# Performance work log

Measured on AMD Instinct MI355X. Metric: run time of the kernel, lower is better.

## Reference

```python
import jax, jax.numpy as jnp
import numpy as np

D_MODEL, D_EDGE, D_STRUCT = 128, 64, 8
N, E, B = 50000, 800000, 1

def _lin(key, din, dout):
    kw, kb = jax.random.split(key)
    s = 1.0 / np.sqrt(din)
    return (jax.random.uniform(kw, (din, dout), jnp.float32, -s, s),
            jax.random.uniform(kb, (dout,), jnp.float32, -s, s))

def setup_inputs() -> dict:
    key = jax.random.key(0)
    ks = jax.random.split(key, 16)
    H = jax.random.normal(ks[0], (B, N, D_MODEL), jnp.float32)
    xyz = jax.random.normal(ks[1], (B, N, 3), jnp.float32)
    edge_index = jax.random.randint(ks[2], (2, E), 0, N, jnp.int64)
    edge_struct = jax.random.normal(ks[3], (E, D_STRUCT), jnp.float32)
    edge_rest_lengths = jax.random.uniform(ks[4], (E,), jnp.float32)
    We1, be1 = _lin(ks[5], 2 * D_MODEL + 2 + D_STRUCT, D_EDGE)
    We2, be2 = _lin(ks[6], D_EDGE, D_EDGE)
    Wg1, bg1 = _lin(ks[7], 2 + D_STRUCT, 32)
    Wg2, bg2 = _lin(ks[8], 32, 1)
    Wn1, bn1 = _lin(ks[9], D_MODEL + D_EDGE, 2 * D_MODEL)
    Wn2, bn2 = _lin(ks[10], 2 * D_MODEL, D_MODEL)
    ln_g = jnp.ones((D_MODEL,), jnp.float32)
    ln_b = jnp.zeros((D_MODEL,), jnp.float32)
    return dict(H=H, xyz=xyz, edge_index=edge_index, edge_struct=edge_struct,
                edge_rest_lengths=edge_rest_lengths,
                We1=We1, be1=be1, We2=We2, be2=be2,
                Wg1=Wg1, bg1=bg1, Wg2=Wg2, bg2=bg2,
                Wn1=Wn1, bn1=bn1, Wn2=Wn2, bn2=bn2,
                ln_g=ln_g, ln_b=ln_b)

def reference(H, xyz, edge_index, edge_struct, edge_rest_lengths,
              We1, be1, We2, be2, Wg1, bg1, Wg2, bg2,
              Wn1, bn1, Wn2, bn2, ln_g, ln_b):
    Bn, Nn, d = H.shape
    i, j = edge_index[0], edge_index[1]
    # edge geometry
    diff = xyz[:, i, :] - xyz[:, j, :]                      # (B,E,3)
    dist2 = jnp.sum(diff * diff, axis=-1, keepdims=True)    # (B,E,1)
    dist = jnp.sqrt(dist2 + 1e-9)
    rest = edge_rest_lengths.reshape(1, -1, 1)
    delta = (dist - rest) / (rest + 1e-9)
    struct = jnp.broadcast_to(edge_struct[None], (Bn, edge_struct.shape[0], edge_struct.shape[1]))
    # edge message MLP
    Hi, Hj = H[:, i, :], H[:, j, :]
    e_in = jnp.concatenate([Hi, Hj, dist2, delta, struct], axis=-1)  # (B,E,2d+2+ds)
    e = jax.nn.silu(e_in @ We1 + be1)
    e_msg = jax.nn.silu(e @ We2 + be2)                       # (B,E,d_edge)
    # gate
    g_in = jnp.concatenate([dist2, delta, struct], axis=-1)
    g = jax.nn.sigmoid(jax.nn.silu(g_in @ Wg1 + bg1) @ Wg2 + bg2)  # (B,E,1)
    e_msg = e_msg * g
    # scatter-add aggregate to destination node i
    agg = jnp.zeros((Bn, Nn, e_msg.shape[-1]), H.dtype).at[:, i, :].add(e_msg)
    # node MLP (dropout is identity at eval) + residual + LayerNorm
    n_in = jnp.concatenate([H, agg], axis=-1)
    upd = jax.nn.silu(n_in @ Wn1 + bn1) @ Wn2 + bn2
    x = H + upd
    mu = jnp.mean(x, axis=-1, keepdims=True)
    var = jnp.mean((x - mu) ** 2, axis=-1, keepdims=True)
    return (x - mu) / jnp.sqrt(var + 1e-5) * ln_g + ln_b
```

## Files before the change

kernel.cpp:

```cpp
#include <hip/hip_runtime.h>
#include <stdint.h>

#define N_NODES 50000
#define N_EDGES 800000
#define NODE_TILES 782

#define SE   72
#define SW2  72
#define SPQ  136
#define SN1  200
#define SN2  264
#define SH1  264
#define ATS  32
#define MSTR 68

#define EC_GRID 962
#define EC_CHUNK 13

#define SCAN_B 98

typedef short bf16x8 __attribute__((ext_vector_type(8)));
typedef short short4v __attribute__((ext_vector_type(4)));
typedef unsigned short ushort8 __attribute__((ext_vector_type(8)));
typedef float f32x4  __attribute__((ext_vector_type(4)));

static __device__ __forceinline__ unsigned short f2bf(float f) {
  unsigned int x = __float_as_uint(f);
  unsigned int r = (x + 0x7fffu + ((x >> 16) & 1u)) >> 16;
  return (unsigned short)r;
}
static __device__ __forceinline__ float bf2f(unsigned short u) {
  return __uint_as_float(((unsigned int)u) << 16);
}
static __device__ __forceinline__ float silu_f(float x) {
  return x * __builtin_amdgcn_rcpf(1.0f + __expf(-x));
}
static __device__ __forceinline__ float sigmoid_f(float x) {
  return __builtin_amdgcn_rcpf(1.0f + __expf(-x));
}
static __device__ __forceinline__ unsigned int cvt_pk_bf16(float lo, float hi) {
  unsigned int r;
  asm("v_cvt_pk_bf16_f32 %0, %1, %2" : "=v"(r) : "v"(lo), "v"(hi));
  return r;
}
static __device__ __forceinline__ bf16x8 pack8(float4 u, float4 v) {
  bf16x8 w;
  w[0] = (short)f2bf(u.x); w[1] = (short)f2bf(u.y);
  w[2] = (short)f2bf(u.z); w[3] = (short)f2bf(u.w);
  w[4] = (short)f2bf(v.x); w[5] = (short)f2bf(v.y);
  w[6] = (short)f2bf(v.z); w[7] = (short)f2bf(v.w);
  return w;
}

__global__ void prep_hist(
    const int* __restrict__ eidx,
    const float* __restrict__ We1, const float* __restrict__ be1,
    const float* __restrict__ We2,
    const float* __restrict__ Wn1, const float* __restrict__ Wn2,
    unsigned short* __restrict__ WpqT, unsigned short* __restrict__ We2T,
    unsigned short* __restrict__ Wn1T, unsigned short* __restrict__ Wn2T,
    unsigned short* __restrict__ WrT,
    int* __restrict__ cnt)
{
  const int gid = blockIdx.x * 256 + threadIdx.x;
  const int gsz = gridDim.x * 256;
  for (int i = gid; i < 128 * SPQ; i += gsz) {
    int n = i / SPQ, k = i % SPQ;
    unsigned short v = 0;
    if (k < 128) v = (n < 64) ? f2bf(We1[k * 64 + n]) : f2bf(We1[(128 + k) * 64 + (n - 64)]);
    WpqT[i] = v;
  }
  for (int i = gid; i < 64 * SW2; i += gsz) {
    int n = i / SW2, k = i % SW2;
    We2T[i] = (k < 64) ? f2bf(We2[k * 64 + n]) : (unsigned short)0;
  }
  for (int i = gid; i < 256 * SN1; i += gsz) {
    int n = i / SN1, k = i % SN1;
    Wn1T[i] = (k < 192) ? f2bf(Wn1[k * 256 + n]) : (unsigned short)0;
  }
  for (int i = gid; i < 128 * SN2; i += gsz) {
    int n = i / SN2, k = i % SN2;
    Wn2T[i] = (k < 256) ? f2bf(Wn2[k * 128 + n]) : (unsigned short)0;
  }
  for (int i = gid; i < 64 * 32; i += gsz) {
    int n = i >> 5, k = i & 31;
    float v = 0.f;
    if (k < 2)       v = We1[256 * 64 + n];
    else if (k < 4)  v = We1[257 * 64 + n];
    else if (k < 12) v = We1[(258 + (k - 4)) * 64 + n];
    else if (k == 12) v = be1[n];
    else if (k == 13) { float w = We1[256 * 64 + n]; v = w - bf2f(f2bf(w)); }
    else if (k == 14) { float w = We1[257 * 64 + n]; v = w - bf2f(f2bf(w)); }
    else if (k == 15) { float w = be1[n];            v = w - bf2f(f2bf(w)); }
    WrT[i] = (k < 16) ? f2bf(v) : (unsigned short)0;
  }
  if (gid < N_EDGES) atomicAdd(&cnt[eidx[gid]], 1);
}

__global__ __launch_bounds__(512) void scan_local(
    const int* __restrict__ cnt, int* __restrict__ rowptr,
    int* __restrict__ bsum)
{
  __shared__ int wsum[8], woff[8];
  const int t = threadIdx.x;
  const int idx = blockIdx.x * 512 + t;
  const int lane = t & 63, wid = t >> 6;
  int c = (idx < N_NODES) ? cnt[idx] : 0;
  int v = c;
  #pragma unroll
  for (int o = 1; o < 64; o <<= 1) {
    int u = __shfl_up(v, o);
    if (lane >= o) v += u;
  }
  if (lane == 63) wsum[wid] = v;
  __syncthreads();
  if (t == 0) {
    int a = 0;
    #pragma unroll
    for (int w = 0; w < 8; ++w) { woff[w] = a; a += wsum[w]; }
    bsum[blockIdx.x] = a;
  }
  __syncthreads();
  if (idx < N_NODES) rowptr[idx] = woff[wid] + (v - c);
}

__global__ __launch_bounds__(128) void scan_mid(
    const int* __restrict__ bsum, int* __restrict__ boff)
{
  __shared__ int ws[2];
  const int t = threadIdx.x;
  const int lane = t & 63, wid = t >> 6;
  int c = (t < SCAN_B) ? bsum[t] : 0;
  int v = c;
  #pragma unroll
  for (int o = 1; o < 64; o <<= 1) {
    int u = __shfl_up(v, o);
    if (lane >= o) v += u;
  }
  if (lane == 63) ws[wid] = v;
  __syncthreads();
  int add = (wid == 1) ? ws[0] : 0;
  if (t < SCAN_B) boff[t] = add + (v - c);
}

__global__ __launch_bounds__(512) void scan_add(
    const int* __restrict__ rowptr, const int* __restrict__ boff,
    int* __restrict__ cursor)
{
  const int idx = blockIdx.x * 512 + threadIdx.x;
  if (idx < N_NODES) cursor[idx] = rowptr[idx] + boff[blockIdx.x];
}

__global__ void fill_kernel(const int* __restrict__ eidx,
                            int* __restrict__ cursor, int* __restrict__ order)
{
  int e = blockIdx.x * 256 + threadIdx.x;
  if (e < N_EDGES) {
    int d = eidx[e];
    int pos = atomicAdd(&cursor[d], 1);
    order[pos] = e;
  }
}

__global__ void reorder_kernel(
    const int* __restrict__ eidx, const float* __restrict__ xyz,
    const float* __restrict__ estruct, const float* __restrict__ erest,
    const int* __restrict__ order,
    const float* __restrict__ Wg1, const float* __restrict__ bg1,
    const float* __restrict__ Wg2, const float* __restrict__ bg2,
    float4* __restrict__ metaA, unsigned short* __restrict__ sst,
    int* __restrict__ in_s)
{
  int s = blockIdx.x * 256 + threadIdx.x;
  if (s >= N_EDGES) return;
  int e = order[s];
  int i = eidx[e], j = eidx[N_EDGES + e];
  float dx = xyz[i * 3 + 0] - xyz[j * 3 + 0];
  float dy = xyz[i * 3 + 1] - xyz[j * 3 + 1];
  float dz = xyz[i * 3 + 2] - xyz[j * 3 + 2];
  float d2 = dx * dx + dy * dy + dz * dz;
  float dist = sqrtf(d2 + 1e-9f);
  float rest = erest[e];
  float dl = (dist - rest) / (rest + 1e-9f);
  float4 s0 = *(const float4*)&estruct[e * 8];
  float4 s1 = *(const float4*)&estruct[e * 8 + 4];
  float st[8] = {s0.x, s0.y, s0.z, s0.w, s1.x, s1.y, s1.z, s1.w};
  float gsum = 0.f;
  #pragma unroll
  for (int h = 0; h < 32; ++h) {
    float a = bg1[h] + d2 * Wg1[0 * 32 + h] + dl * Wg1[1 * 32 + h];
    #pragma unroll
    for (int c = 0; c < 8; ++c) a += st[c] * Wg1[(2 + c) * 32 + h];
    gsum += silu_f(a) * Wg2[h];
  }
  float g = sigmoid_f(gsum + bg2[0]);
  metaA[s] = make_float4(d2, dl, g, __int_as_float(j));
  ushort8 w;
  #pragma unroll
  for (int c = 0; c < 8; ++c) w[c] = f2bf(st[c]);
  *(ushort8*)&sst[(long)s * 8] = w;
  in_s[s] = i;
}

__global__ __launch_bounds__(256, 2) void pq_kernel(
    const float* __restrict__ H, const unsigned short* __restrict__ WpqT,
    unsigned short* __restrict__ P, unsigned short* __restrict__ Q,
    unsigned short* __restrict__ Hbf)
{
  __shared__ unsigned short As[64 * SPQ];
  __shared__ unsigned short Ws[128 * SPQ];

  const int tid  = threadIdx.x;
  const int lane = tid & 63;
  const int wv   = tid >> 6;
  const int lr   = lane & 15;
  const int lq   = lane >> 4;
  const int m0   = wv * 16;
  const int n0   = blockIdx.x * 64;

  for (int i = tid * 8; i < 128 * SPQ; i += 256 * 8)
    *(bf16x8*)&Ws[i] = *(const bf16x8*)&WpqT[i];
  {
    int le = tid >> 2, q = tid & 3;
    int node = n0 + le; if (node >= N_NODES) node = N_NODES - 1;
    const float* src = H + (long)node * 128 + q * 32;
    unsigned short* dst = &As[le * SPQ + q * 32];
    #pragma unroll
    for (int c = 0; c < 32; c += 8) {
      float4 u = *(const float4*)(src + c);
      float4 v = *(const float4*)(src + c + 4);
      *(bf16x8*)(dst + c) = pack8(u, v);
    }
  }
  __syncthreads();

  for (int idx = tid * 8; idx < 64 * 128; idx += 256 * 8) {
    int row = idx >> 7, col = idx & 127;
    *(bf16x8*)&Hbf[((long)n0 + row) * 128 + col] = *(const bf16x8*)&As[row * SPQ + col];
  }

  f32x4 zero4 = {0.f, 0.f, 0.f, 0.f};
  f32x4 acc[8];
  #pragma unroll
  for (int f = 0; f < 8; ++f) acc[f] = zero4;
  #pragma unroll
  for (int s = 0; s < 4; ++s) {
    int kb = s * 32 + lq * 8;
    bf16x8 a = *(const bf16x8*)&As[(m0 + lr) * SPQ + kb];
    #pragma unroll
    for (int f = 0; f < 8; ++f) {
      bf16x8 b = *(const bf16x8*)&Ws[(f * 16 + lr) * SPQ + kb];
      acc[f] = __builtin_amdgcn_mfma_f32_16x16x32_bf16(a, b, acc[f], 0, 0, 0);
    }
  }
  #pragma unroll
  for (int f = 0; f < 8; ++f) {
    #pragma unroll
    for (int r = 0; r < 4; ++r) {
      int node = n0 + m0 + lq * 4 + r;
      if (node < N_NODES) {
        if (f < 4) P[(long)node * 64 + f * 16 + lr] = f2bf(acc[f][r]);
        else       Q[(long)node * 64 + (f - 4) * 16 + lr] = f2bf(acc[f][r]);
      }
    }
  }
}

__global__ __launch_bounds__(256, 4) void edge_compute(
    const unsigned short* __restrict__ P, const unsigned short* __restrict__ Q,
    const int* __restrict__ in_s,
    const float4* __restrict__ metaA, const unsigned short* __restrict__ sst,
    const unsigned short* __restrict__ We2T, const float* __restrict__ be2,
    const unsigned short* __restrict__ WrT,
    float* __restrict__ agg)
{
  __shared__ unsigned short W2s[64 * SW2];
  __shared__ unsigned short Es [4 * 16 * SE];
  __shared__ unsigned short At [4 * 16 * ATS];
  __shared__ float          Ms [4 * 16 * MSTR];

  const int tid  = threadIdx.x;
  const int lane = tid & 63;
  const int wv   = tid >> 6;
  const int lr   = lane & 15;
  const int lq   = lane >> 4;

  for (int i = tid * 8; i < 64 * SW2; i += 256 * 8)
    *(bf16x8*)&W2s[i] = *(const bf16x8*)&We2T[i];

  unsigned short* Es_w = &Es[wv * 16 * SE];
  unsigned short* At_w = &At[wv * 16 * ATS];
  float*          Ms_w = &Ms[wv * 16 * MSTR];

  if (lane < 16) {
    ushort8 z;
    #pragma unroll
    for (int c = 0; c < 8; ++c) z[c] = 0;
    *(ushort8*)&At_w[lane * ATS + 16] = z;
    *(ushort8*)&At_w[lane * ATS + 24] = z;
  }

  bf16x8 aWr[4];
  float bias2[4][4];
  #pragma unroll
  for (int f = 0; f < 4; ++f) {
    aWr[f] = *(const bf16x8*)&WrT[(f * 16 + lr) * 32 + lq * 8];
    #pragma unroll
    for (int r = 0; r < 4; ++r) bias2[f][r] = be2[f * 16 + lq * 4 + r];
  }
  __syncthreads();

  const int n_tiles = N_EDGES / 16;
  const int wid = blockIdx.x * 4 + wv;
  const int t0 = wid * EC_CHUNK;
  const int t1 = (t0 + EC_CHUNK < n_tiles) ? (t0 + EC_CHUNK) : n_tiles;
  if (t0 >= n_tiles) return;

  f32x4 zero4 = {0.f, 0.f, 0.f, 0.f};
  int   cur_node   = in_s[t0 * 16];
  float acc        = 0.f;
  bool  use_atomic = true;

  for (int tile = t0; tile < t1; ++tile) {
    const int s0 = tile * 16;

    float4 mm = metaA[s0 + lr];
    int   inode = in_s[s0 + lr];
    int   jnode = __float_as_int(mm.w);
    float g     = mm.z;

    if (lane < 16) {
      ushort8 sv = *(const ushort8*)&sst[(long)(s0 + lane) * 8];
      float d2 = mm.x, dl = mm.y;
      unsigned short d2h = f2bf(d2);
      unsigned short d2l = f2bf(d2 - bf2f(d2h));
      unsigned short dlh = f2bf(dl);
      unsigned short dll = f2bf(dl - bf2f(dlh));
      ushort8 w0, w1;
      w0[0] = d2h;   w0[1] = d2l;   w0[2] = dlh;   w0[3] = dll;
      w0[4] = sv[0]; w0[5] = sv[1]; w0[6] = sv[2]; w0[7] = sv[3];
      w1[0] = sv[4]; w1[1] = sv[5]; w1[2] = sv[6]; w1[3] = sv[7];
      w1[4] = 0x3F80u; w1[5] = d2h; w1[6] = dlh;  w1[7] = 0x3F80u;
      *(ushort8*)&At_w[lane * ATS]     = w0;
      *(ushort8*)&At_w[lane * ATS + 8] = w1;
    }

    bf16x8 bA = *(const bf16x8*)&At_w[lr * ATS + lq * 8];
    f32x4 acc1[4];
    #pragma unroll
    for (int f = 0; f < 4; ++f)
      acc1[f] = __builtin_amdgcn_mfma_f32_16x16x32_bf16(aWr[f], bA, zero4, 0, 0, 0);

    const unsigned short* Pb = P + (long)inode * 64;
    const unsigned short* Qb = Q + (long)jnode * 64;
    #pragma unroll
    for (int f = 0; f < 4; ++f) {
      short4v pv = *(const short4v*)&Pb[f * 16 + lq * 4];
      short4v qv = *(const short4v*)&Qb[f * 16 + lq * 4];
      float v0 = silu_f(bf2f((unsigned short)pv[0]) + bf2f((unsigned short)qv[0]) + acc1[f][0]);
      float v1 = silu_f(bf2f((unsigned short)pv[1]) + bf2f((unsigned short)qv[1]) + acc1[f][1]);
      float v2 = silu_f(bf2f((unsigned short)pv[2]) + bf2f((unsigned short)qv[2]) + acc1[f][2]);
      float v3 = silu_f(bf2f((unsigned short)pv[3]) + bf2f((unsigned short)qv[3]) + acc1[f][3]);
      uint2 w;
      w.x = cvt_pk_bf16(v0, v1);
      w.y = cvt_pk_bf16(v2, v3);
      *(uint2*)&Es_w[lr * SE + f * 16 + lq * 4] = w;
    }

    f32x4 acc2[4];
    #pragma unroll
    for (int f = 0; f < 4; ++f) acc2[f] = zero4;
    #pragma unroll
    for (int s = 0; s < 2; ++s) {
      int kb = s * 32 + lq * 8;
      bf16x8 bE = *(const bf16x8*)&Es_w[lr * SE + kb];
      #pragma unroll
      for (int f = 0; f < 4; ++f) {
        bf16x8 aW = *(const bf16x8*)&W2s[(f * 16 + lr) * SW2 + kb];
        acc2[f] = __builtin_amdgcn_mfma_f32_16x16x32_bf16(aW, bE, acc2[f], 0, 0, 0);
      }
    }

    #pragma unroll
    for (int f = 0; f < 4; ++f) {
      f32x4 o;
      o[0] = silu_f(acc2[f][0] + bias2[f][0]) * g;
      o[1] = silu_f(acc2[f][1] + bias2[f][1]) * g;
      o[2] = silu_f(acc2[f][2] + bias2[f][2]) * g;
      o[3] = silu_f(acc2[f][3] + bias2[f][3]) * g;
      *(f32x4*)&Ms_w[lr * MSTR + f * 16 + lq * 4] = o;
    }

    #pragma unroll
    for (int e = 0; e < 16; ++e) {
      int ie = __builtin_amdgcn_readlane(inode, e);
      if (ie != cur_node) {
        if (use_atomic) atomicAdd(&agg[(long)cur_node * 64 + lane], acc);
        else            agg[(long)cur_node * 64 + lane] = acc;
        use_atomic = false;
        cur_node = ie;
        acc = 0.f;
      }
      acc += Ms_w[e * MSTR + lane];
    }
  }
  atomicAdd(&agg[(long)cur_node * 64 + lane], acc);
}

__global__ __launch_bounds__(256, 4) void node_fused_kernel(
    const float* __restrict__ H, const unsigned short* __restrict__ Hbf,
    const float* __restrict__ agg,
    const unsigned short* __restrict__ Wn1T, const float* __restrict__ bn1,
    const unsigned short* __restrict__ Wn2T, const float* __restrict__ bn2,
    const float* __restrict__ ln_g, const float* __restrict__ ln_b,
    float* __restrict__ out)
{
  __shared__ unsigned short h1t[64 * SH1];

  const int tid  = threadIdx.x;
  const int lane = tid & 63;
  const int wv   = tid >> 6;
  const int lr   = lane & 15;
  const int lq   = lane >> 4;
  const int m0   = wv * 16;
  const int n0   = blockIdx.x * 64;

  int rowa = n0 + m0 + lr;
  int rowc = rowa < N_NODES ? rowa : N_NODES - 1;

  f32x4 zero4 = {0.f, 0.f, 0.f, 0.f};
  f32x4 acc1[16];
  #pragma unroll
  for (int f = 0; f < 16; ++f) acc1[f] = zero4;
  #pragma unroll
  for (int s = 0; s < 6; ++s) {
    int kb = s * 32 + lq * 8;
    bf16x8 a;
    if (s < 4) {
      a = *(const bf16x8*)&Hbf[(long)rowa * 128 + kb];
    } else {
      const float* p = agg + (long)rowc * 64 + (kb - 128);
      float4 u = *(const float4*)p;
      float4 v = *(const float4*)(p + 4);
      a = pack8(u, v);
    }
    #pragma unroll
    for (int f = 0; f < 16; ++f) {
      bf16x8 b = *(const bf16x8*)&Wn1T[(long)(f * 16 + lr) * SN1 + kb];
      acc1[f] = __builtin_amdgcn_mfma_f32_16x16x32_bf16(a, b, acc1[f], 0, 0, 0);
    }
  }
  #pragma unroll
  for (int f = 0; f < 16; ++f) {
    float bias = bn1[f * 16 + lr];
    #pragma unroll
    for (int r = 0; r < 4; ++r)
      h1t[(m0 + lq * 4 + r) * SH1 + f * 16 + lr] = f2bf(silu_f(acc1[f][r] + bias));
  }

  f32x4 acc2[8];
  #pragma unroll
  for (int f = 0; f < 8; ++f) acc2[f] = zero4;
  #pragma unroll
  for (int s = 0; s < 8; ++s) {
    int kb = s * 32 + lq * 8;
    bf16x8 a = *(const bf16x8*)&h1t[(m0 + lr) * SH1 + kb];
    #pragma unroll
    for (int f = 0; f < 8; ++f) {
      bf16x8 b = *(const bf16x8*)&Wn2T[(long)(f * 16 + lr) * SN2 + kb];
      acc2[f] = __builtin_amdgcn_mfma_f32_16x16x32_bf16(a, b, acc2[f], 0, 0, 0);
    }
  }

  #pragma unroll
  for (int r = 0; r < 4; ++r) {
    int node = n0 + m0 + lq * 4 + r;
    int nc = node < N_NODES ? node : N_NODES - 1;
    float x[8];
    float sum = 0.f, sumsq = 0.f;
    #pragma unroll
    for (int f = 0; f < 8; ++f) {
      int n = f * 16 + lr;
      float u = acc2[f][r] + bn2[n];
      float xv = H[(long)nc * 128 + n] + u;
      x[f] = xv;
      sum += xv;
      sumsq += xv * xv;
    }
    #pragma unroll
    for (int o = 1; o < 16; o <<= 1) {
      sum   += __shfl_xor(sum, o);
      sumsq += __shfl_xor(sumsq, o);
    }
    float mu  = sum * (1.f / 128.f);
    float var = sumsq * (1.f / 128.f) - mu * mu;
    float rstd = rsqrtf(var + 1e-5f);
    if (node < N_NODES) {
      #pragma unroll
      for (int f = 0; f < 8; ++f) {
        int n = f * 16 + lr;
        out[(long)node * 128 + n] = (x[f] - mu) * rstd * ln_g[n] + ln_b[n];
      }
    }
  }
}

extern "C" void kernel_launch(void* const* d_in, const int* in_sizes, int n_in,
                              void* d_out, int out_size, void* d_ws, size_t ws_size,
                              hipStream_t stream) {
  const float* H       = (const float*)d_in[0];
  const float* xyz     = (const float*)d_in[1];
  const int*   eidx    = (const int*)d_in[2];
  const float* estruct = (const float*)d_in[3];
  const float* erest   = (const float*)d_in[4];
  const float* We1     = (const float*)d_in[5];
  const float* be1     = (const float*)d_in[6];
  const float* We2     = (const float*)d_in[7];
  const float* be2     = (const float*)d_in[8];
  const float* Wg1     = (const float*)d_in[9];
  const float* bg1     = (const float*)d_in[10];
  const float* Wg2     = (const float*)d_in[11];
  const float* bg2     = (const float*)d_in[12];
  const float* Wn1     = (const float*)d_in[13];
  const float* bn1     = (const float*)d_in[14];
  const float* Wn2     = (const float*)d_in[15];
  const float* bn2     = (const float*)d_in[16];
  const float* ln_g    = (const float*)d_in[17];
  const float* ln_b    = (const float*)d_in[18];

  char* ws = (char*)d_ws;
  float*          agg    = (float*)(ws + 0);
  unsigned short* Hbf    = (unsigned short*)(ws + 12812288);
  float4*         metaA  = (float4*)(ws + 25624576);
  unsigned short* sst    = (unsigned short*)(ws + 38424576);
  int*            in_s   = (int*)(ws + 51224576);
  int*            order  = (int*)(ws + 54424576);
  unsigned short* P      = (unsigned short*)(ws + 54424576);
  unsigned short* Qm     = (unsigned short*)(ws + 60824576);
  int*            cnt    = (int*)(ws + 67224576);
  int*            rowptr = (int*)(ws + 67424768);
  int*            cursor = (int*)(ws + 67624960);
  unsigned short* WpqT   = (unsigned short*)(ws + 67825152);
  unsigned short* We2T   = (unsigned short*)(ws + 67859968);
  unsigned short* Wn1T   = (unsigned short*)(ws + 67869184);
  unsigned short* Wn2T   = (unsigned short*)(ws + 67971584);
  unsigned short* WrT    = (unsigned short*)(ws + 68039168);
  int*            bsum   = (int*)(ws + 68043264);
  int*            boff   = (int*)(ws + 68043776);
  float* out = (float*)d_out;

  hipMemsetAsync(cnt, 0, (size_t)N_NODES * sizeof(int), stream);
  hipMemsetAsync(agg, 0, (size_t)50048 * 64 * sizeof(float), stream);

  hipLaunchKernelGGL(prep_hist, dim3(3125), dim3(256), 0, stream,
                     eidx, We1, be1, We2, Wn1, Wn2, WpqT, We2T, Wn1T, Wn2T, WrT, cnt);
  hipLaunchKernelGGL(scan_local, dim3(SCAN_B), dim3(512), 0, stream,
                     cnt, rowptr, bsum);
  hipLaunchKernelGGL(scan_mid, dim3(1), dim3(128), 0, stream,
                     bsum, boff);
  hipLaunchKernelGGL(scan_add, dim3(SCAN_B), dim3(512), 0, stream,
                     rowptr, boff, cursor);
  hipLaunchKernelGGL(fill_kernel, dim3(3125), dim3(256), 0, stream,
                     eidx, cursor, order);
  hipLaunchKernelGGL(reorder_kernel, dim3(3125), dim3(256), 0, stream,
                     eidx, xyz, estruct, erest, order,
                     Wg1, bg1, Wg2, bg2, metaA, sst, in_s);
  hipLaunchKernelGGL(pq_kernel, dim3(NODE_TILES), dim3(256), 0, stream,
                     H, WpqT, P, Qm, Hbf);
  hipLaunchKernelGGL(edge_compute, dim3(EC_GRID), dim3(256), 0, stream,
                     P, Qm, in_s, metaA, sst, We2T, be2, WrT, agg);
  hipLaunchKernelGGL(node_fused_kernel, dim3(NODE_TILES), dim3(256), 0, stream,
                     H, Hbf, agg, Wn1T, bn1, Wn2T, bn2, ln_g, ln_b, out);
}
```

Baseline: 402.0 us.

## Fuse fill into reorder, bf16 message staging, split node MLP with LDS weights

Merges the edge fill and reorder kernels so each edge computes its gate and writes directly to its CSR slot via an atomic cursor, removing the order array pass. Edge messages are staged in LDS as bf16 instead of fp32, halving shared traffic. The fused node MLP is split into two persistent kernels that keep Wn1 halves and Wn2 in LDS, with h1 round-tripped through global memory. This adds an extra global write and read of h1 and changes the edge order within each segment to be nondeterministic.

Result: faster. 389.7 us (-3.1%).

```diff
diff --git a/kernel.cpp b/kernel.cpp
--- a/kernel.cpp
+++ b/kernel.cpp
@@ -8,11 +8,10 @@
 #define SE   72
 #define SW2  72
 #define SPQ  136
-#define SN1  200
-#define SN2  264
-#define SH1  264
-#define ATS  32
-#define MSTR 68
+#define SN1  216
+#define SN2  280
+#define ATS  40
+#define MSTR 72
 
 #define EC_GRID 962
 #define EC_CHUNK 13
@@ -151,29 +150,17 @@
   if (idx < N_NODES) cursor[idx] = rowptr[idx] + boff[blockIdx.x];
 }
 
-__global__ void fill_kernel(const int* __restrict__ eidx,
-                            int* __restrict__ cursor, int* __restrict__ order)
-{
-  int e = blockIdx.x * 256 + threadIdx.x;
-  if (e < N_EDGES) {
-    int d = eidx[e];
-    int pos = atomicAdd(&cursor[d], 1);
-    order[pos] = e;
-  }
-}
-
-__global__ void reorder_kernel(
+__global__ void fill_reorder(
     const int* __restrict__ eidx, const float* __restrict__ xyz,
     const float* __restrict__ estruct, const float* __restrict__ erest,
-    const int* __restrict__ order,
+    int* __restrict__ cursor,
     const float* __restrict__ Wg1, const float* __restrict__ bg1,
     const float* __restrict__ Wg2, const float* __restrict__ bg2,
     float4* __restrict__ metaA, unsigned short* __restrict__ sst,
     int* __restrict__ in_s)
 {
-  int s = blockIdx.x * 256 + threadIdx.x;
-  if (s >= N_EDGES) return;
-  int e = order[s];
+  int e = blockIdx.x * 256 + threadIdx.x;
+  if (e >= N_EDGES) return;
   int i = eidx[e], j = eidx[N_EDGES + e];
   float dx = xyz[i * 3 + 0] - xyz[j * 3 + 0];
   float dy = xyz[i * 3 + 1] - xyz[j * 3 + 1];
@@ -194,12 +181,14 @@
     gsum += silu_f(a) * Wg2[h];
   }
   float g = sigmoid_f(gsum + bg2[0]);
-  metaA[s] = make_float4(d2, dl, g, __int_as_float(j));
+
+  int pos = atomicAdd(&cursor[i], 1);
+  metaA[pos] = make_float4(d2, dl, g, __int_as_float(j));
   ushort8 w;
   #pragma unroll
   for (int c = 0; c < 8; ++c) w[c] = f2bf(st[c]);
-  *(ushort8*)&sst[(long)s * 8] = w;
-  in_s[s] = i;
+  *(ushort8*)&sst[(long)pos * 8] = w;
+  in_s[pos] = i;
 }
 
 __global__ __launch_bounds__(256, 2) void pq_kernel(
@@ -277,7 +266,7 @@
   __shared__ unsigned short W2s[64 * SW2];
   __shared__ unsigned short Es [4 * 16 * SE];
   __shared__ unsigned short At [4 * 16 * ATS];
-  __shared__ float          Ms [4 * 16 * MSTR];
+  __shared__ unsigned short Ms [4 * 16 * MSTR];
 
   const int tid  = threadIdx.x;
   const int lane = tid & 63;
@@ -290,7 +279,7 @@
 
   unsigned short* Es_w = &Es[wv * 16 * SE];
   unsigned short* At_w = &At[wv * 16 * ATS];
-  float*          Ms_w = &Ms[wv * 16 * MSTR];
+  unsigned short* Ms_w = &Ms[wv * 16 * MSTR];
 
   if (lane < 16) {
     ushort8 z;
@@ -383,12 +372,14 @@
 
     #pragma unroll
     for (int f = 0; f < 4; ++f) {
-      f32x4 o;
-      o[0] = silu_f(acc2[f][0] + bias2[f][0]) * g;
-      o[1] = silu_f(acc2[f][1] + bias2[f][1]) * g;
-      o[2] = silu_f(acc2[f][2] + bias2[f][2]) * g;
-      o[3] = silu_f(acc2[f][3] + bias2[f][3]) * g;
-      *(f32x4*)&Ms_w[lr * MSTR + f * 16 + lq * 4] = o;
+      float o0 = silu_f(acc2[f][0] + bias2[f][0]) * g;
+      float o1 = silu_f(acc2[f][1] + bias2[f][1]) * g;
+      float o2 = silu_f(acc2[f][2] + bias2[f][2]) * g;
+      float o3 = silu_f(acc2[f][3] + bias2[f][3]) * g;
+      uint2 w;
+      w.x = cvt_pk_bf16(o0, o1);
+      w.y = cvt_pk_bf16(o2, o3);
+      *(uint2*)&Ms_w[lr * MSTR + f * 16 + lq * 4] = w;
     }
 
     #pragma unroll
@@ -401,21 +392,18 @@
         cur_node = ie;
         acc = 0.f;
       }
-      acc += Ms_w[e * MSTR + lane];
+      acc += bf2f(Ms_w[e * MSTR + lane]);
     }
   }
   atomicAdd(&agg[(long)cur_node * 64 + lane], acc);
 }
 
-__global__ __launch_bounds__(256, 4) void node_fused_kernel(
-    const float* __restrict__ H, const unsigned short* __restrict__ Hbf,
-    const float* __restrict__ agg,
+__global__ __launch_bounds__(256, 2) void h1_kernel(
+    const unsigned short* __restrict__ Hbf, const float* __restrict__ agg,
     const unsigned short* __restrict__ Wn1T, const float* __restrict__ bn1,
-    const unsigned short* __restrict__ Wn2T, const float* __restrict__ bn2,
-    const float* __restrict__ ln_g, const float* __restrict__ ln_b,
-    float* __restrict__ out)
-{
-  __shared__ unsigned short h1t[64 * SH1];
+    unsigned short* __restrict__ h1)
+{
+  __shared__ unsigned short Wl[128 * SN1];
 
   const int tid  = threadIdx.x;
   const int lane = tid & 63;
@@ -423,83 +411,119 @@
   const int lr   = lane & 15;
   const int lq   = lane >> 4;
   const int m0   = wv * 16;
-  const int n0   = blockIdx.x * 64;
-
-  int rowa = n0 + m0 + lr;
-  int rowc = rowa < N_NODES ? rowa : N_NODES - 1;
+  const int p    = blockIdx.x & 1;
+
+  for (int i = tid * 8; i < 128 * SN1; i += 256 * 8)
+    *(bf16x8*)&Wl[i] = *(const bf16x8*)&Wn1T[p * 128 * SN1 + i];
+  __syncthreads();
 
   f32x4 zero4 = {0.f, 0.f, 0.f, 0.f};
-  f32x4 acc1[16];
-  #pragma unroll
-  for (int f = 0; f < 16; ++f) acc1[f] = zero4;
-  #pragma unroll
-  for (int s = 0; s < 6; ++s) {
-    int kb = s * 32 + lq * 8;
-    bf16x8 a;
-    if (s < 4) {
-      a = *(const bf16x8*)&Hbf[(long)rowa * 128 + kb];
-    } else {
-      const float* p = agg + (long)rowc * 64 + (kb - 128);
-      float4 u = *(const float4*)p;
-      float4 v = *(const float4*)(p + 4);
-      a = pack8(u, v);
-    }
-    #pragma unroll
-    for (int f = 0; f < 16; ++f) {
-      bf16x8 b = *(const bf16x8*)&Wn1T[(long)(f * 16 + lr) * SN1 + kb];
-      acc1[f] = __builtin_amdgcn_mfma_f32_16x16x32_bf16(a, b, acc1[f], 0, 0, 0);
-    }
-  }
-  #pragma unroll
-  for (int f = 0; f < 16; ++f) {
-    float bias = bn1[f * 16 + lr];
-    #pragma unroll
-    for (int r = 0; r < 4; ++r)
-      h1t[(m0 + lq * 4 + r) * SH1 + f * 16 + lr] = f2bf(silu_f(acc1[f][r] + bias));
-  }
-
-  f32x4 acc2[8];
-  #pragma unroll
-  for (int f = 0; f < 8; ++f) acc2[f] = zero4;
-  #pragma unroll
-  for (int s = 0; s < 8; ++s) {
-    int kb = s * 32 + lq * 8;
-    bf16x8 a = *(const bf16x8*)&h1t[(m0 + lr) * SH1 + kb];
+  for (int t = blockIdx.x >> 1; t < NODE_TILES; t += 256) {
+    const int n0 = t * 64;
+    int rowa = n0 + m0 + lr;
+    int rowc = rowa < N_NODES ? rowa : N_NODES - 1;
+
+    f32x4 acc1[8];
+    #pragma unroll
+    for (int f = 0; f < 8; ++f) acc1[f] = zero4;
+    #pragma unroll
+    for (int s = 0; s < 6; ++s) {
+      int kb = s * 32 + lq * 8;
+      bf16x8 a;
+      if (s < 4) {
+        a = *(const bf16x8*)&Hbf[(long)rowa * 128 + kb];
+      } else {
+        const float* pp = agg + (long)rowc * 64 + (kb - 128);
+        float4 u = *(const float4*)pp;
+        float4 v = *(const float4*)(pp + 4);
+        a = pack8(u, v);
+      }
+      #pragma unroll
+      for (int f = 0; f < 8; ++f) {
+        bf16x8 b = *(const bf16x8*)&Wl[(f * 16 + lr) * SN1 + kb];
+        acc1[f] = __builtin_amdgcn_mfma_f32_16x16x32_bf16(a, b, acc1[f], 0, 0, 0);
+      }
+    }
     #pragma unroll
     for (int f = 0; f < 8; ++f) {
-      bf16x8 b = *(const bf16x8*)&Wn2T[(long)(f * 16 + lr) * SN2 + kb];
-      acc2[f] = __builtin_amdgcn_mfma_f32_16x16x32_bf16(a, b, acc2[f], 0, 0, 0);
-    }
-  }
-
-  #pragma unroll
-  for (int r = 0; r < 4; ++r) {
-    int node = n0 + m0 + lq * 4 + r;
-    int nc = node < N_NODES ? node : N_NODES - 1;
-    float x[8];
-    float sum = 0.f, sumsq = 0.f;
-    #pragma unroll
-    for (int f = 0; f < 8; ++f) {
-      int n = f * 16 + lr;
-      float u = acc2[f][r] + bn2[n];
-      float xv = H[(long)nc * 128 + n] + u;
-      x[f] = xv;
-      sum += xv;
-      sumsq += xv * xv;
-    }
-    #pragma unroll
-    for (int o = 1; o < 16; o <<= 1) {
-      sum   += __shfl_xor(sum, o);
-      sumsq += __shfl_xor(sumsq, o);
-    }
-    float mu  = sum * (1.f / 128.f);
-    float var = sumsq * (1.f / 128.f) - mu * mu;
-    float rstd = rsqrtf(var + 1e-5f);
-    if (node < N_NODES) {
+      int col = p * 128 + f * 16 + lr;
+      float bias = bn1[col];
+      #pragma unroll
+      for (int r = 0; r < 4; ++r) {
+        int node = n0 + m0 + lq * 4 + r;
+        h1[(long)node * 256 + col] = f2bf(silu_f(acc1[f][r] + bias));
+      }
+    }
+  }
+}
+
+__global__ __launch_bounds__(256, 2) void out_kernel(
+    const float* __restrict__ H, const unsigned short* __restrict__ h1,
+    const unsigned short* __restrict__ Wn2T, const float* __restrict__ bn2,
+    const float* __restrict__ ln_g, const float* __restrict__ ln_b,
+    float* __restrict__ out)
+{
+  __shared__ unsigned short Wl[128 * SN2];
+
+  const int tid  = threadIdx.x;
+  const int lane = tid & 63;
+  const int wv   = tid >> 6;
+  const int lr   = lane & 15;
+  const int lq   = lane >> 4;
+  const int m0   = wv * 16;
+
+  for (int i = tid * 8; i < 128 * SN2; i += 256 * 8)
+    *(bf16x8*)&Wl[i] = *(const bf16x8*)&Wn2T[i];
+  __syncthreads();
+
+  f32x4 zero4 = {0.f, 0.f, 0.f, 0.f};
+  for (int t = blockIdx.x; t < NODE_TILES; t += 512) {
+    const int n0 = t * 64;
+    int rowa = n0 + m0 + lr;
+
+    f32x4 acc2[8];
+    #pragma unroll
+    for (int f = 0; f < 8; ++f) acc2[f] = zero4;
+    #pragma unroll
+    for (int s = 0; s < 8; ++s) {
+      int kb = s * 32 + lq * 8;
+      bf16x8 a = *(const bf16x8*)&h1[(long)rowa * 256 + kb];
+      #pragma unroll
+      for (int f = 0; f < 8; ++f) {
+        bf16x8 b = *(const bf16x8*)&Wl[(f * 16 + lr) * SN2 + kb];
+        acc2[f] = __builtin_amdgcn_mfma_f32_16x16x32_bf16(a, b, acc2[f], 0, 0, 0);
+      }
+    }
+
+    #pragma unroll
+    for (int r = 0; r < 4; ++r) {
+      int node = n0 + m0 + lq * 4 + r;
+      int nc = node < N_NODES ? node : N_NODES - 1;
+      float x[8];
+      float sum = 0.f, sumsq = 0.f;
       #pragma unroll
       for (int f = 0; f < 8; ++f) {
         int n = f * 16 + lr;
-        out[(long)node * 128 + n] = (x[f] - mu) * rstd * ln_g[n] + ln_b[n];
+        float u = acc2[f][r] + bn2[n];
+        float xv = H[(long)nc * 128 + n] + u;
+        x[f] = xv;
+        sum += xv;
+        sumsq += xv * xv;
+      }
+      #pragma unroll
+      for (int o = 1; o < 16; o <<= 1) {
+        sum   += __shfl_xor(sum, o);
+        sumsq += __shfl_xor(sumsq, o);
+      }
+      float mu  = sum * (1.f / 128.f);
+      float var = sumsq * (1.f / 128.f) - mu * mu;
+      float rstd = rsqrtf(var + 1e-5f);
+      if (node < N_NODES) {
+        #pragma unroll
+        for (int f = 0; f < 8; ++f) {
+          int n = f * 16 + lr;
+          out[(long)node * 128 + n] = (x[f] - mu) * rstd * ln_g[n] + ln_b[n];
+        }
       }
     }
   }
@@ -534,7 +558,6 @@
   float4*         metaA  = (float4*)(ws + 25624576);
   unsigned short* sst    = (unsigned short*)(ws + 38424576);
   int*            in_s   = (int*)(ws + 51224576);
-  int*            order  = (int*)(ws + 54424576);
   unsigned short* P      = (unsigned short*)(ws + 54424576);
   unsigned short* Qm     = (unsigned short*)(ws + 60824576);
   int*            cnt    = (int*)(ws + 67224576);
@@ -542,11 +565,12 @@
   int*            cursor = (int*)(ws + 67624960);
   unsigned short* WpqT   = (unsigned short*)(ws + 67825152);
   unsigned short* We2T   = (unsigned short*)(ws + 67859968);
-  unsigned short* Wn1T   = (unsigned short*)(ws + 67869184);
-  unsigned short* Wn2T   = (unsigned short*)(ws + 67971584);
-  unsigned short* WrT    = (unsigned short*)(ws + 68039168);
-  int*            bsum   = (int*)(ws + 68043264);
-  int*            boff   = (int*)(ws + 68043776);
+  unsigned short* Wn1T   = (unsigned short*)(ws + 67871232);
+  unsigned short* Wn2T   = (unsigned short*)(ws + 67981824);
+  unsigned short* WrT    = (unsigned short*)(ws + 68053504);
+  int*            bsum   = (int*)(ws + 68057600);
+  int*            boff   = (int*)(ws + 68058112);
+  unsigned short* h1     = (unsigned short*)(ws + 68058624);
   float* out = (float*)d_out;
 
   hipMemsetAsync(cnt, 0, (size_t)N_NODES * sizeof(int), stream);
@@ -560,15 +584,15 @@
                      bsum, boff);
   hipLaunchKernelGGL(scan_add, dim3(SCAN_B), dim3(512), 0, stream,
                      rowptr, boff, cursor);
-  hipLaunchKernelGGL(fill_kernel, dim3(3125), dim3(256), 0, stream,
-                     eidx, cursor, order);
-  hipLaunchKernelGGL(reorder_kernel, dim3(3125), dim3(256), 0, stream,
-                     eidx, xyz, estruct, erest, order,
+  hipLaunchKernelGGL(fill_reorder, dim3(3125), dim3(256), 0, stream,
+                     eidx, xyz, estruct, erest, cursor,
                      Wg1, bg1, Wg2, bg2, metaA, sst, in_s);
   hipLaunchKernelGGL(pq_kernel, dim3(NODE_TILES), dim3(256), 0, stream,
                      H, WpqT, P, Qm, Hbf);
   hipLaunchKernelGGL(edge_compute, dim3(EC_GRID), dim3(256), 0, stream,
                      P, Qm, in_s, metaA, sst, We2T, be2, WrT, agg);
-  hipLaunchKernelGGL(node_fused_kernel, dim3(NODE_TILES), dim3(256), 0, stream,
-                     H, Hbf, agg, Wn1T, bn1, Wn2T, bn2, ln_g, ln_b, out);
-}
+  hipLaunchKernelGGL(h1_kernel, dim3(512), dim3(256), 0, stream,
+                     Hbf, agg, Wn1T, bn1, h1);
+  hipLaunchKernelGGL(out_kernel, dim3(512), dim3(256), 0, stream,
+                     H, h1, Wn2T, bn2, ln_g, ln_b, out);
+}
```
